# Kernel tuning notes

Hardware: AMD Instinct MI355X
Metric: run time of the kernel (lower is better)

## Reference

```python
import jax, jax.numpy as jnp
import numpy as np

B, S, D, H = 2, 2048, 1024, 16
HD = D // H  # 64


def setup_inputs() -> dict:
    key = jax.random.key(0)
    k0, k1, k2 = jax.random.split(key, 3)
    return {
        "x": jax.random.normal(k0, (B, S, D), jnp.float32),
        "qkv_w": jax.random.normal(k1, (D, 3 * D), jnp.float32) / np.sqrt(D).astype(np.float32),
        "qkv_b": jnp.zeros((3 * D,), jnp.float32),
        "out_w": jax.random.normal(k2, (D, D), jnp.float32) / np.sqrt(D).astype(np.float32),
        "out_b": jnp.zeros((D,), jnp.float32),
    }


def reference(x, qkv_w, qkv_b, out_w, out_b):
    b, s, d = x.shape
    h, hd = H, d // H
    scale = 1.0 / np.sqrt(hd).astype(np.float32)
    # qkv projection: [b, s, 3d] -> [b, s, 3, h, hd]
    qkv = (x @ qkv_w + qkv_b).reshape(b, s, 3, h, hd)
    q, k, v = qkv[:, :, 0], qkv[:, :, 1], qkv[:, :, 2]  # each [b, s, h, hd]
    # attention logits [b, h, q, k]
    logits = jnp.einsum("bqhd,bkhd->bhqk", q, k)
    # causal mask applied before scaling (as in source; -inf is scale-invariant)
    causal_mask = jnp.triu(jnp.ones((s, s), bool), 1)
    logits = jnp.where(causal_mask, -jnp.inf, logits) * scale
    att = jax.nn.softmax(logits, axis=-1)
    out = jnp.einsum("bhqk,bkhd->bqhd", att, v).reshape(b, s, d)
    return out @ out_w + out_b
```

## Files before the change

### kernel.cpp

```cpp
#include <hip/hip_runtime.h>


typedef __bf16 bf16x8 __attribute__((ext_vector_type(8)));
typedef float f32x4 __attribute__((ext_vector_type(4)));
typedef float f32x16 __attribute__((ext_vector_type(16)));
typedef unsigned short u16;
typedef u16 u16x8 __attribute__((ext_vector_type(8)));
typedef unsigned u32x4 __attribute__((ext_vector_type(4)));

#define NEG_INF (-__builtin_inff())
#define QSCALE 0.180336880110323f
#define FIXED_M 24.0f

__device__ __forceinline__ u16 f2b(float f) {
    unsigned u = __builtin_bit_cast(unsigned, f);
    u += 0x7fffu + ((u >> 16) & 1u);
    return (u16)(u >> 16);
}

__device__ __forceinline__ unsigned cvtpk(float lo, float hi) {
    unsigned r;
    asm("v_cvt_pk_bf16_f32 %0, %1, %2" : "=v"(r) : "v"(lo), "v"(hi));
    return r;
}

__device__ __forceinline__ void plswap(unsigned &a, unsigned &b) {
    asm("v_permlane32_swap_b32 %0, %1" : "+v"(a), "+v"(b));
}

__device__ __forceinline__ void gload_lds16(const u16* g, u16* l) {
    __builtin_amdgcn_global_load_lds(
        (__attribute__((address_space(1))) unsigned int*)(g),
        (__attribute__((address_space(3))) unsigned int*)(l),
        16u, 0, 0u);
}

__device__ __forceinline__ int swzb(int u) {
    return u ^ (((u >> 7) & 7) << 4);
}

__global__ void cast_f32_bf16(const float* __restrict__ X, u16* __restrict__ Y, int n4)
{
    int i = blockIdx.x * blockDim.x + threadIdx.x;
    if (i >= n4) return;
    float4 v = ((const float4*)X)[i];
    ((ushort4*)Y)[i] = make_ushort4(f2b(v.x), f2b(v.y), f2b(v.z), f2b(v.w));
}

__global__ void transpose_cast(const float* __restrict__ W, u16* __restrict__ Wt, int K, int N)
{
    __shared__ float tile[32][33];
    const int c0 = blockIdx.x * 32, r0 = blockIdx.y * 32;
    const int tc = threadIdx.x & 31, tr = threadIdx.x >> 5;
#pragma unroll
    for (int i = 0; i < 4; ++i)
        tile[tr + i*8][tc] = W[(size_t)(r0 + tr + i*8) * N + c0 + tc];
    __syncthreads();
#pragma unroll
    for (int i = 0; i < 4; ++i) {
        int nn = tr + i*8;
        Wt[(size_t)(c0 + nn) * K + r0 + tc] = f2b(tile[tc][nn]);
    }
}

template<int MODE>
__global__ __launch_bounds__(256) void gemm_bt(
    const u16* __restrict__ A, const u16* __restrict__ Bt,
    const float* __restrict__ bias, float* __restrict__ Cf,
    u16* __restrict__ qb, u16* __restrict__ kb, u16* __restrict__ vb,
    int M, int N, int K)
{
    __shared__ __align__(16) u16 As[2][128 * 32];
    __shared__ __align__(16) u16 Bs[2][128 * 32];
    const int tid  = threadIdx.x;
    const int wave = tid >> 6, lane = tid & 63;
    const int quad = lane >> 4, l16 = lane & 15;

    const int nx = gridDim.x, nwg = nx * gridDim.y;
    int wg = blockIdx.y * nx + blockIdx.x;
    wg = (wg & 7) * (nwg >> 3) + (wg >> 3);
    const int m0 = (wg / nx) * 128, n0 = (wg % nx) * 128;
    const int wm = (wave >> 1) * 64, wn = (wave & 1) * 64;

    f32x4 acc[4][4] = {};

    auto stage = [&](int buf, int kt) {
#pragma unroll
        for (int iss = 0; iss < 2; ++iss) {
            const int e = iss * 2048 + tid * 8;
            const int row = e >> 5, col = e & 31;
            gload_lds16(A  + (size_t)(m0 + row) * K + kt + col, &As[buf][iss * 2048 + wave * 512]);
            gload_lds16(Bt + (size_t)(n0 + row) * K + kt + col, &Bs[buf][iss * 2048 + wave * 512]);
        }
    };

    stage(0, 0);
    __syncthreads();

    int buf = 0;
    for (int kt = 0; kt < K; kt += 32) {
        if (kt + 32 < K) stage(buf ^ 1, kt + 32);

        bf16x8 af[4], bfr[4];
#pragma unroll
        for (int i = 0; i < 4; ++i) {
            af[i]  = *(const bf16x8*)(&As[buf][(wm + i*16 + l16) * 32 + quad * 8]);
            bfr[i] = *(const bf16x8*)(&Bs[buf][(wn + i*16 + l16) * 32 + quad * 8]);
        }
#pragma unroll
        for (int i = 0; i < 4; ++i)
#pragma unroll
            for (int j = 0; j < 4; ++j)
                acc[i][j] = __builtin_amdgcn_mfma_f32_16x16x32_bf16(af[i], bfr[j], acc[i][j], 0, 0, 0);
        __syncthreads();
        buf ^= 1;
    }

#pragma unroll
    for (int i = 0; i < 4; ++i)
#pragma unroll
        for (int j = 0; j < 4; ++j)
#pragma unroll
            for (int r = 0; r < 4; ++r) {
                const int m = m0 + wm + i*16 + quad*4 + r;
                const int n = n0 + wn + j*16 + l16;
                float v = acc[i][j][r] + bias[n];
                if (MODE == 0) {
                    Cf[(size_t)m * N + n] = v;
                } else {
                    const int t = n >> 10, h = (n >> 6) & 15, hd = n & 63;
                    const int b = m >> 11, s = m & 2047;
                    const size_t idx = ((size_t)(b * 16 + h) * 2048 + s) * 64 + hd;
                    if (t == 0)      qb[idx] = f2b(v * QSCALE);
                    else if (t == 1) kb[idx] = f2b(v);
                    else             vb[idx] = f2b(v);
                }
            }
}

__global__ __launch_bounds__(256) void transpose_v(const u16* __restrict__ vb, u16* __restrict__ vt)
{
    __shared__ u16 tile[64][72];
    const int bh = blockIdx.y, s0 = blockIdx.x * 64;
    const size_t base = (size_t)bh * (2048 * 64);
    const int r = threadIdx.x >> 3, c = (threadIdx.x & 7) * 8;
#pragma unroll
    for (int i = 0; i < 2; ++i) {
        u16x8 v = *(const u16x8*)(vb + base + (size_t)(s0 + r + i*32) * 64 + c);
        *(u16x8*)(&tile[r + i*32][c]) = v;
    }
    __syncthreads();
#pragma unroll
    for (int i = 0; i < 2; ++i) {
        const int hd = r + i*32;
        u16 tmp[8];
#pragma unroll
        for (int j = 0; j < 8; ++j) tmp[j] = tile[c + j][hd];
        *(u16x8*)(vt + base + (size_t)hd * 2048 + s0 + c) = *(u16x8*)&tmp[0];
    }
}

__global__ __launch_bounds__(256) void flash_attn(
    const u16* __restrict__ qb, const u16* __restrict__ kb, const u16* __restrict__ vt,
    u16* __restrict__ attn)
{
    __shared__ __align__(16) u16 Kl[2][4096];
    __shared__ __align__(16) u16 Vl[2][4096];
    __shared__ float red_f[2][2][2][16][64];
    __shared__ float red_li[2][2][64];
    __shared__ float al[2][2][32];

    const int tid  = threadIdx.x;
    const int wave = tid >> 6, lane = tid & 63;
    const int l31 = lane & 31, hi = lane >> 5;
    const int hi8 = hi * 8, hi4 = hi * 4;

    const int lin = (int)blockIdx.x;
    const int bh  = (lin & 7) | (((lin >> 3) & 3) << 3);
    const int g   = lin >> 5;
    const int pairsel = wave >> 1, phase = wave & 1;
    const int p   = 2 * g + pairsel;
    const size_t base = (size_t)bh * (2048 * 64);

    const int rb0 = 32 * p;
    const int rb1 = 32 * (63 - p);
    const int klo = p, khi = 63 - p;
    const int T = 32 - g;

    int koff[2], voff[2], dstw[2];
#pragma unroll
    for (int i = 0; i < 2; ++i) {
        const int u = (tid + 256 * i) * 16;
        const int ktsub = u >> 12, krow = (u >> 7) & 31;
        koff[i] = (ktsub * 32 + krow) * 64 + ((u & 127) >> 1);
        const int half = (u >> 6) & 1;
        voff[i] = (krow * 2 + half) * 2048 + ktsub * 32 + ((u & 63) >> 1);
        dstw[i] = swzb(u) >> 1;
    }
    int rdK[4], rdV[2][2];
#pragma unroll
    for (int ks = 0; ks < 4; ++ks) {
        const int u = phase * 4096 + l31 * 128 + ks * 32 + hi * 16;
        rdK[ks] = swzb(u) >> 1;
    }
#pragma unroll
    for (int c = 0; c < 2; ++c)
#pragma unroll
        for (int s2 = 0; s2 < 2; ++s2) {
            const int u = phase * 4096 + (c * 16 + (l31 >> 1)) * 128 + (l31 & 1) * 64
                        + s2 * 32 + hi * 16;
            rdV[c][s2] = swzb(u) >> 1;
        }

    bf16x8 qf[2][4];
#pragma unroll
    for (int ks = 0; ks < 4; ++ks) {
        qf[0][ks] = *(const bf16x8*)(qb + base + (size_t)(rb0 + l31) * 64 + ks*16 + hi8);
        qf[1][ks] = *(const bf16x8*)(qb + base + (size_t)(rb1 + l31) * 64 + ks*16 + hi8);
    }

    f32x16 minit;
#pragma unroll
    for (int r = 0; r < 16; ++r) minit[r] = -FIXED_M;

    f32x16 of[2][2] = {};
    float li[2] = {0.f, 0.f};

    u16x8 rk[2], rv[2];
    auto LOADS = [&](int s) {
#pragma unroll
        for (int i = 0; i < 2; ++i) {
            rk[i] = *(const u16x8*)(kb + base + (size_t)s * 4096 + koff[i]);
            rv[i] = *(const u16x8*)(vt + base + (size_t)s * 64 + voff[i]);
        }
    };
    auto WRITES = [&](int b) {
#pragma unroll
        for (int i = 0; i < 2; ++i) {
            *(u16x8*)(&Kl[b][dstw[i]]) = rk[i];
            *(u16x8*)(&Vl[b][dstw[i]]) = rv[i];
        }
    };

    LOADS(0); WRITES(0);
    __syncthreads();

    for (int s = 0; s < T; ++s) {
        const bool pre = (s + 1 < T);
        if (pre) LOADS(s + 1);

        const int kth = 2 * s + phase;
        const int key0 = kth * 32;
        const bool a_hi = (kth <= khi), a_lo = (kth <= klo);

        if (a_hi | a_lo) {
            const int buf = s & 1;
            bf16x8 kf[4], vf[2][2];
#pragma unroll
            for (int ks = 0; ks < 4; ++ks)
                kf[ks] = *(const bf16x8*)(&Kl[buf][rdK[ks]]);
#pragma unroll
            for (int c = 0; c < 2; ++c)
#pragma unroll
                for (int s2 = 0; s2 < 2; ++s2)
                    vf[c][s2] = *(const bf16x8*)(&Vl[buf][rdV[c][s2]]);

#define PROC_TILE(TT, RB, MT)                                                    \
        do {                                                                     \
            __builtin_amdgcn_s_setprio(1);                                       \
            f32x16 st = __builtin_amdgcn_mfma_f32_32x32x16_bf16(kf[0], qf[TT][0], minit, 0, 0, 0); \
            _Pragma("unroll")                                                    \
            for (int ks = 1; ks < 4; ++ks)                                       \
                st = __builtin_amdgcn_mfma_f32_32x32x16_bf16(kf[ks], qf[TT][ks], st, 0, 0, 0); \
            __builtin_amdgcn_s_setprio(0);                                       \
            const bool mt_ = (MT);                                               \
            const int lim_ = (RB) + l31 - key0;                                  \
            _Pragma("unroll")                                                    \
            for (int r = 0; r < 16; ++r) {                                       \
                float e = __builtin_exp2f(st[r]);                                \
                if (mt_ && ((r&3) + 8*(r>>2) + hi4 > lim_)) e = 0.f;             \
                st[r] = e;                                                       \
            }                                                                    \
            li[TT] += (((st[0]+st[1]) + (st[2]+st[3])) + ((st[4]+st[5]) + (st[6]+st[7]))) \
                    + (((st[8]+st[9]) + (st[10]+st[11])) + ((st[12]+st[13]) + (st[14]+st[15]))); \
            unsigned cw[8];                                                      \
            _Pragma("unroll")                                                    \
            for (int i = 0; i < 8; ++i) cw[i] = cvtpk(st[2*i], st[2*i+1]);       \
            plswap(cw[0], cw[2]); plswap(cw[1], cw[3]);                          \
            plswap(cw[4], cw[6]); plswap(cw[5], cw[7]);                          \
            bf16x8 pa[2];                                                        \
            { u32x4 t0 = {cw[0], cw[1], cw[2], cw[3]};                           \
              u32x4 t1 = {cw[4], cw[5], cw[6], cw[7]};                           \
              pa[0] = __builtin_bit_cast(bf16x8, t0);                            \
              pa[1] = __builtin_bit_cast(bf16x8, t1); }                          \
            __builtin_amdgcn_s_setprio(1);                                       \
            _Pragma("unroll")                                                    \
            for (int c = 0; c < 2; ++c) {                                        \
                of[TT][c] = __builtin_amdgcn_mfma_f32_32x32x16_bf16(pa[0], vf[c][0], of[TT][c], 0, 0, 0); \
                of[TT][c] = __builtin_amdgcn_mfma_f32_32x32x16_bf16(pa[1], vf[c][1], of[TT][c], 0, 0, 0); \
            }                                                                    \
            __builtin_amdgcn_s_setprio(0);                                       \
        } while (0)

            if (a_hi) PROC_TILE(1, rb1, kth == khi);
            if (a_lo) PROC_TILE(0, rb0, kth == klo);
#undef PROC_TILE
        }

        if (pre) WRITES((s + 1) & 1);
        __syncthreads();
    }

    if (phase) {
#pragma unroll
        for (int t = 0; t < 2; ++t) {
#pragma unroll
            for (int c = 0; c < 2; ++c)
#pragma unroll
                for (int i = 0; i < 16; ++i)
                    red_f[pairsel][t][c][i][lane] = of[t][c][i];
            red_li[pairsel][t][lane] = li[t];
        }
    }
    __syncthreads();
    if (phase) return;
#pragma unroll
    for (int t = 0; t < 2; ++t) {
#pragma unroll
        for (int c = 0; c < 2; ++c)
#pragma unroll
            for (int i = 0; i < 16; ++i)
                of[t][c][i] += red_f[pairsel][t][c][i][lane];
        li[t] += red_li[pairsel][t][lane];
    }

#pragma unroll
    for (int t = 0; t < 2; ++t) {
        li[t] += __shfl_xor(li[t], 32);
        al[pairsel][t][l31] = li[t];
    }
    const int b = bh >> 4, h = bh & 15;
    const int rbs[2] = {rb0, rb1};
#pragma unroll
    for (int t = 0; t < 2; ++t)
#pragma unroll
        for (int gq = 0; gq < 4; ++gq) {
            const f32x4 lv = *(const f32x4*)(&al[pairsel][t][gq*8 + hi4]);
            f32x4 inv;
#pragma unroll
            for (int rr = 0; rr < 4; ++rr) inv[rr] = 1.0f / lv[rr];
#pragma unroll
            for (int c = 0; c < 2; ++c)
#pragma unroll
                for (int rr = 0; rr < 4; ++rr) {
                    const int q = rbs[t] + gq*8 + hi4 + rr;
                    u16* dst = attn + ((size_t)(b * 2048 + q)) * 1024 + h * 64 + c*32;
                    dst[l31] = f2b(of[t][c][gq*4 + rr] * inv[rr]);
                }
        }
}

extern "C" void kernel_launch(void* const* d_in, const int* in_sizes, int n_in,
                              void* d_out, int out_size, void* d_ws, size_t ws_size,
                              hipStream_t stream)
{
    const float* x     = (const float*)d_in[0];
    const float* qkv_w = (const float*)d_in[1];
    const float* qkv_b = (const float*)d_in[2];
    const float* out_w = (const float*)d_in[3];
    const float* out_b = (const float*)d_in[4];
    float* out = (float*)d_out;

    char* ws = (char*)d_ws;
    u16* qkv_wt = (u16*)ws;  ws += (size_t)3072 * 1024 * 2;
    u16* out_wt = (u16*)ws;  ws += (size_t)1024 * 1024 * 2;
    u16* xb     = (u16*)ws;  ws += (size_t)4096 * 1024 * 2;
    u16* qb     = (u16*)ws;  ws += (size_t)4096 * 1024 * 2;
    u16* kb     = (u16*)ws;  ws += (size_t)4096 * 1024 * 2;
    u16* vb     = (u16*)ws;  ws += (size_t)4096 * 1024 * 2;
    u16* vt     = (u16*)ws;

    cast_f32_bf16<<<4096, 256, 0, stream>>>(x, xb, 4096 * 1024 / 4);
    transpose_cast<<<dim3(96, 32), 256, 0, stream>>>(qkv_w, qkv_wt, 1024, 3072);
    transpose_cast<<<dim3(32, 32), 256, 0, stream>>>(out_w, out_wt, 1024, 1024);

    gemm_bt<1><<<dim3(24, 32), 256, 0, stream>>>(xb, qkv_wt, qkv_b, nullptr,
                                                 qb, kb, vb, 4096, 3072, 1024);
    transpose_v<<<dim3(32, 32), 256, 0, stream>>>(vb, vt);
    flash_attn<<<512, 256, 0, stream>>>(qb, kb, vt, xb);
    gemm_bt<0><<<dim3(8, 32), 256, 0, stream>>>(xb, out_wt, out_b, out,
                                                nullptr, nullptr, nullptr, 4096, 1024, 1024);
}
```

Before: 194.0 us.

## Use 256x256-tile 512-thread pipelined GEMM for QKV projection

Replaces the 128x128-tile QKV projection GEMM with a dedicated 256x256-tile kernel using 8 waves. It uses a two-stage split-K LDS double buffer with direct global-to-LDS loads, explicit waitcnt/barrier scheduling and setprio around the MFMA bursts. This raises arithmetic intensity per loaded byte and overlaps loads with MFMAs, at the cost of more LDS and registers per workgroup and only 192 workgroups. It also remaps the flash-attention block-to-head assignment, likely for cache or XCD locality.

After: 201.9 us. +4.1%, slower.

```diff
diff --git a/kernel.cpp b/kernel.cpp
--- a/kernel.cpp
+++ b/kernel.cpp
@@ -8,7 +8,6 @@
 typedef u16 u16x8 __attribute__((ext_vector_type(8)));
 typedef unsigned u32x4 __attribute__((ext_vector_type(4)));
 
-#define NEG_INF (-__builtin_inff())
 #define QSCALE 0.180336880110323f
 #define FIXED_M 24.0f
 
@@ -63,11 +62,103 @@
     }
 }
 
-template<int MODE>
-__global__ __launch_bounds__(256) void gemm_bt(
+__global__ __launch_bounds__(512) void gemm256_qkv(
+    const u16* __restrict__ A, const u16* __restrict__ Bt,
+    const float* __restrict__ bias,
+    u16* __restrict__ qb, u16* __restrict__ kb, u16* __restrict__ vb)
+{
+    __shared__ __align__(16) u16 Asl[2][2][256 * 32];
+    __shared__ __align__(16) u16 Bsl[2][2][256 * 32];
+    const int tid  = threadIdx.x;
+    const int wave = tid >> 6, lane = tid & 63;
+    const int quad = lane >> 4, l16 = lane & 15;
+    const int wr = wave >> 2, wc = wave & 3;
+    const int m0 = blockIdx.y * 256, n0 = blockIdx.x * 256;
+
+    int srow[2], scol[2];
+#pragma unroll
+    for (int i = 0; i < 2; ++i) {
+        const int off = i * 8192 + tid * 16;
+        srow[i] = off >> 6;
+        scol[i] = (off & 63) >> 1;
+    }
+    const int ldst0 = (wave * 1024) >> 1;
+    const int ldst1 = (8192 + wave * 1024) >> 1;
+
+    auto STA = [&](int nb, int kh, int kt) {
+        gload_lds16(A + (size_t)(m0 + srow[0]) * 1024 + kt + kh*32 + scol[0], &Asl[nb][kh][ldst0]);
+        gload_lds16(A + (size_t)(m0 + srow[1]) * 1024 + kt + kh*32 + scol[1], &Asl[nb][kh][ldst1]);
+    };
+    auto STB = [&](int nb, int kh, int kt) {
+        gload_lds16(Bt + (size_t)(n0 + srow[0]) * 1024 + kt + kh*32 + scol[0], &Bsl[nb][kh][ldst0]);
+        gload_lds16(Bt + (size_t)(n0 + srow[1]) * 1024 + kt + kh*32 + scol[1], &Bsl[nb][kh][ldst1]);
+    };
+
+    f32x4 acc[8][4] = {};
+    bf16x8 bfr[4];
+
+    STA(0, 0, 0); STB(0, 0, 0); STA(0, 1, 0); STB(0, 1, 0);
+
+#define GPHASE(S, H, STAGE)                                                      \
+    {                                                                            \
+        bf16x8 af[4];                                                            \
+        _Pragma("unroll")                                                        \
+        for (int f = 0; f < 4; ++f)                                              \
+            af[f] = *(const bf16x8*)(&Asl[buf][S][(wr*128 + (H)*64 + f*16 + l16)*32 + quad*8]); \
+        if ((H) == 0) {                                                          \
+            _Pragma("unroll")                                                    \
+            for (int nf = 0; nf < 4; ++nf)                                       \
+                bfr[nf] = *(const bf16x8*)(&Bsl[buf][S][(wc*64 + nf*16 + l16)*32 + quad*8]); \
+        }                                                                        \
+        STAGE;                                                                   \
+        __builtin_amdgcn_s_setprio(1);                                           \
+        _Pragma("unroll")                                                        \
+        for (int f = 0; f < 4; ++f)                                              \
+            _Pragma("unroll")                                                    \
+            for (int nf = 0; nf < 4; ++nf)                                       \
+                acc[(H)*4 + f][nf] = __builtin_amdgcn_mfma_f32_16x16x32_bf16(    \
+                    af[f], bfr[nf], acc[(H)*4 + f][nf], 0, 0, 0);                \
+        __builtin_amdgcn_s_setprio(0);                                           \
+    }
+
+    for (int t = 0; t < 16; ++t) {
+        const int buf = t & 1, nbuf = buf ^ 1;
+        const int ktn = (t < 15 ? t + 1 : 15) * 64;
+        asm volatile("s_waitcnt vmcnt(4)" ::: "memory");
+        __builtin_amdgcn_s_barrier();
+        __builtin_amdgcn_sched_barrier(0);
+        GPHASE(0, 0, STA(nbuf, 0, ktn));
+        GPHASE(0, 1, STB(nbuf, 0, ktn));
+        asm volatile("s_waitcnt vmcnt(4)" ::: "memory");
+        __builtin_amdgcn_s_barrier();
+        __builtin_amdgcn_sched_barrier(0);
+        GPHASE(1, 0, STA(nbuf, 1, ktn));
+        GPHASE(1, 1, STB(nbuf, 1, ktn));
+    }
+#undef GPHASE
+    asm volatile("s_waitcnt vmcnt(0)" ::: "memory");
+
+#pragma unroll
+    for (int mf = 0; mf < 8; ++mf)
+#pragma unroll
+        for (int nf = 0; nf < 4; ++nf)
+#pragma unroll
+            for (int r = 0; r < 4; ++r) {
+                const int m = m0 + wr*128 + mf*16 + quad*4 + r;
+                const int n = n0 + wc*64 + nf*16 + l16;
+                float v = acc[mf][nf][r] + bias[n];
+                const int tt = n >> 10, h = (n >> 6) & 15, hd = n & 63;
+                const int b = m >> 11, s = m & 2047;
+                const size_t idx = ((size_t)(b*16 + h) * 2048 + s) * 64 + hd;
+                if (tt == 0)      qb[idx] = f2b(v * QSCALE);
+                else if (tt == 1) kb[idx] = f2b(v);
+                else              vb[idx] = f2b(v);
+            }
+}
+
+__global__ __launch_bounds__(256) void gemm_proj(
     const u16* __restrict__ A, const u16* __restrict__ Bt,
     const float* __restrict__ bias, float* __restrict__ Cf,
-    u16* __restrict__ qb, u16* __restrict__ kb, u16* __restrict__ vb,
     int M, int N, int K)
 {
     __shared__ __align__(16) u16 As[2][128 * 32];
@@ -124,17 +215,7 @@
             for (int r = 0; r < 4; ++r) {
                 const int m = m0 + wm + i*16 + quad*4 + r;
                 const int n = n0 + wn + j*16 + l16;
-                float v = acc[i][j][r] + bias[n];
-                if (MODE == 0) {
-                    Cf[(size_t)m * N + n] = v;
-                } else {
-                    const int t = n >> 10, h = (n >> 6) & 15, hd = n & 63;
-                    const int b = m >> 11, s = m & 2047;
-                    const size_t idx = ((size_t)(b * 16 + h) * 2048 + s) * 64 + hd;
-                    if (t == 0)      qb[idx] = f2b(v * QSCALE);
-                    else if (t == 1) kb[idx] = f2b(v);
-                    else             vb[idx] = f2b(v);
-                }
+                Cf[(size_t)m * N + n] = acc[i][j][r] + bias[n];
             }
 }
 
@@ -176,7 +257,7 @@
     const int hi8 = hi * 8, hi4 = hi * 4;
 
     const int lin = (int)blockIdx.x;
-    const int bh  = (lin & 7) | (((lin >> 3) & 3) << 3);
+    const int bh  = 2*(lin & 7) + ((lin >> 3) & 1) + 16*((lin >> 4) & 1);
     const int g   = lin >> 5;
     const int pairsel = wave >> 1, phase = wave & 1;
     const int p   = 2 * g + pairsel;
@@ -384,10 +465,8 @@
     transpose_cast<<<dim3(96, 32), 256, 0, stream>>>(qkv_w, qkv_wt, 1024, 3072);
     transpose_cast<<<dim3(32, 32), 256, 0, stream>>>(out_w, out_wt, 1024, 1024);
 
-    gemm_bt<1><<<dim3(24, 32), 256, 0, stream>>>(xb, qkv_wt, qkv_b, nullptr,
-                                                 qb, kb, vb, 4096, 3072, 1024);
+    gemm256_qkv<<<dim3(12, 16), 512, 0, stream>>>(xb, qkv_wt, qkv_b, qb, kb, vb);
     transpose_v<<<dim3(32, 32), 256, 0, stream>>>(vb, vt);
     flash_attn<<<512, 256, 0, stream>>>(qb, kb, vt, xb);
-    gemm_bt<0><<<dim3(8, 32), 256, 0, stream>>>(xb, out_wt, out_b, out,
-                                                nullptr, nullptr, nullptr, 4096, 1024, 1024);
-}
+    gemm_proj<<<dim3(8, 32), 256, 0, stream>>>(xb, out_wt, out_b, out, 4096, 1024, 1024);
+}
```
